# Kernel tuning notes

Hardware: AMD Instinct MI355X
Metric: run time of the kernel (lower is better)

The kernel has to match this reference:

```python
import jax, jax.numpy as jnp
import numpy as np

N_NODES = 100000
N_EDGES = 1600000
N_FEAT = 128
HIDDEN = 64
N_CLASSES = 16


def setup_inputs() -> dict:
    key = jax.random.key(0)
    ks = jax.random.split(key, 8)
    x = jax.random.normal(ks[0], (N_NODES, N_FEAT), dtype=jnp.float32)
    edge_index = jax.random.randint(ks[1], (2, N_EDGES), 0, N_NODES, dtype=jnp.int64)
    def glorot(k, shape):
        lim = float(np.sqrt(6.0 / (shape[0] + shape[1])))
        return jax.random.uniform(k, shape, jnp.float32, -lim, lim)
    return {
        "x": x,
        "edge_index": edge_index,
        "W0": glorot(ks[2], (N_FEAT, HIDDEN)), "b0": jnp.zeros((HIDDEN,), jnp.float32),
        "W1": glorot(ks[3], (HIDDEN, HIDDEN)), "b1": jnp.zeros((HIDDEN,), jnp.float32),
        "W2": glorot(ks[4], (HIDDEN, 2)),      "b2": jnp.zeros((2,), jnp.float32),
        "Wc": glorot(ks[5], (2, N_CLASSES)),   "bc": jnp.zeros((N_CLASSES,), jnp.float32),
    }


def _gcn_conv(x, W, b, src, dst, norm, n_nodes):
    # GCNConv: D^{-1/2} (A + I) D^{-1/2} X W + b, edges already include self-loops
    h = x @ W                                  # transform first (small dim)
    msg = h[src] * norm[:, None]               # gather + per-edge scale
    agg = jax.ops.segment_sum(msg, dst, num_segments=n_nodes)  # scatter-add
    return agg + b


def reference(x, edge_index, W0, b0, W1, b1, W2, b2, Wc, bc):
    n = x.shape[0]
    loops = jnp.arange(n, dtype=edge_index.dtype)
    src = jnp.concatenate([edge_index[0], loops])
    dst = jnp.concatenate([edge_index[1], loops])
    # degree on destination (col), including self-loops
    deg = jax.ops.segment_sum(jnp.ones_like(dst, dtype=x.dtype), dst, num_segments=n)
    dis = jnp.where(deg > 0, jax.lax.rsqrt(deg), 0.0)
    norm = dis[src] * dis[dst]

    h = _gcn_conv(x, W0, b0, src, dst, norm, n)              # layer 0, no activation
    h = jnp.tanh(_gcn_conv(h, W1, b1, src, dst, norm, n))    # layer 1
    h = jnp.tanh(_gcn_conv(h, W2, b2, src, dst, norm, n))    # layer 2 -> [N, 2]
    embeddings = h
    out = embeddings @ Wc + bc                               # [N, num_classes]
    return (out, embeddings)
```

## Files before the change

kernel.cpp:

```cpp
#include <hip/hip_runtime.h>


#define NF 128
#define NH 64
#define NPB 256
#define MAXNB 512
#define CAP 6144
#define A1G 1024

__global__ void k_init0(const int* __restrict__ ei, int* __restrict__ fmt,
                        int* __restrict__ ccnt, int nb16) {
    int i = blockIdx.x * 256 + threadIdx.x;
    if (i < nb16) ccnt[i] = 0;
    if (i == 0) {
        int f = 1;
        #pragma unroll
        for (int k = 1; k < 32; k += 2) if (ei[k] != 0) f = 0;
        *fmt = f;
    }
}

__global__ void __launch_bounds__(256) k_coarse(
        const int* __restrict__ ei, const int* __restrict__ fmt,
        int* __restrict__ ccnt, int* __restrict__ blockbase, int E, int NB) {
    __shared__ int h[MAXNB];
    int sh = *fmt;
    for (int i = threadIdx.x; i < NB; i += 256) h[i] = 0;
    __syncthreads();
    for (long long e = (long long)blockIdx.x * 256 + threadIdx.x; e < E;
         e += (long long)A1G * 256) {
        int d = ei[(long long)(E + e) << sh];
        atomicAdd(&h[d >> 8], 1);
    }
    __syncthreads();
    for (int b = threadIdx.x; b < NB; b += 256) {
        int c = h[b];
        int base = (c > 0) ? atomicAdd(&ccnt[b * 16], c) : 0;
        blockbase[(long long)blockIdx.x * NB + b] = base;
    }
}

__global__ void __launch_bounds__(512) k_cscan(
        const int* __restrict__ ccnt, int* __restrict__ cstart, int NB) {
    __shared__ int s[512];
    int t = threadIdx.x;
    int c = (t < NB) ? ccnt[t * 16] : 0;
    s[t] = c;
    __syncthreads();
    for (int off = 1; off < 512; off <<= 1) {
        int v = s[t];
        int u = (t >= off) ? s[t - off] : 0;
        __syncthreads();
        s[t] = v + u;
        __syncthreads();
    }
    if (t < NB) cstart[t] = s[t] - c;
}

__global__ void __launch_bounds__(256) k_cscatter(
        const int* __restrict__ ei, const int* __restrict__ fmt,
        const int* __restrict__ cstart, const int* __restrict__ blockbase,
        int* __restrict__ pairs, int E, int NB) {
    __shared__ int h[MAXNB];
    __shared__ int bb[MAXNB];
    int sh = *fmt;
    for (int i = threadIdx.x; i < NB; i += 256) {
        h[i] = 0;
        bb[i] = cstart[i] + blockbase[(long long)blockIdx.x * NB + i];
    }
    __syncthreads();
    for (long long e = (long long)blockIdx.x * 256 + threadIdx.x; e < E;
         e += (long long)A1G * 256) {
        int s = ei[(long long)e << sh];
        int d = ei[(long long)(E + e) << sh];
        int b = d >> 8;
        int r = atomicAdd(&h[b], 1);
        pairs[bb[b] + r] = s | ((d & 255) << 17);
    }
}

__global__ void __launch_bounds__(256) k_bucket(
        const int* __restrict__ pairs, const int* __restrict__ ccnt,
        const int* __restrict__ cstart, int* __restrict__ esrc,
        int* __restrict__ cnt, int* __restrict__ start, float* __restrict__ dis,
        int N) {
    __shared__ int words[CAP];
    __shared__ unsigned char rk[CAP];
    __shared__ int h[NPB];
    __shared__ int hs[NPB];
    int b = blockIdx.x;
    int cs = cstart[b];
    int ec = ccnt[b * 16];
    if (ec > CAP) ec = CAP;
    int t = threadIdx.x;
    for (int i = t; i < ec; i += 256) words[i] = pairs[cs + i];
    h[t] = 0;
    __syncthreads();
    for (int i = t; i < ec; i += 256) {
        int ld = words[i] >> 17;
        rk[i] = (unsigned char)atomicAdd(&h[ld], 1);
    }
    __syncthreads();
    int c = h[t];
    hs[t] = c;
    __syncthreads();
    for (int off = 1; off < 256; off <<= 1) {
        int v = hs[t];
        int u = (t >= off) ? hs[t - off] : 0;
        __syncthreads();
        hs[t] = v + u;
        __syncthreads();
    }
    int node = b * NPB + t;
    if (node < N) {
        cnt[node] = c;
        start[node] = cs + hs[t] - c;
        dis[node] = rsqrtf(1.0f + (float)c);
    }
    for (int i = t; i < ec; i += 256) {
        int w = words[i];
        int ld = w >> 17;
        esrc[cs + (hs[ld] - h[ld]) + rk[i]] = w & 0x1FFFF;
    }
}

template<int K>
__global__ void __launch_bounds__(256) k_gemm(
        const float* __restrict__ X, const float* __restrict__ W,
        const float* __restrict__ dis, short* __restrict__ T16,
        float* __restrict__ rs, int n) {
    constexpr int KP = K + 4;
    __shared__ float xs[64 * KP];
    __shared__ float Ws[K * NH];
    __shared__ int rmax[64];
    if (threadIdx.x < 64) rmax[threadIdx.x] = 0;
    for (int i = threadIdx.x; i < K * NH / 4; i += 256)
        ((float4*)Ws)[i] = ((const float4*)W)[i];
    long long rowbase = (long long)blockIdx.x * 64;
    const float4* X4 = (const float4*)(X + rowbase * K);
    long long lim4 = ((long long)n * K - rowbase * K) >> 2;
    for (int i = threadIdx.x; i < 16 * K; i += 256) {
        float4 v = (i < lim4) ? X4[i] : make_float4(0.f, 0.f, 0.f, 0.f);
        int r = i / (K / 4), kk = (i % (K / 4)) * 4;
        *(float4*)&xs[r * KP + kk] = v;
    }
    __syncthreads();
    int c0 = (threadIdx.x & 15) * 4;
    int r0 = (threadIdx.x >> 4) * 4;
    const float* x0 = &xs[(r0 + 0) * KP];
    const float* x1 = &xs[(r0 + 1) * KP];
    const float* x2 = &xs[(r0 + 2) * KP];
    const float* x3 = &xs[(r0 + 3) * KP];
    float4 a0{0,0,0,0}, a1{0,0,0,0}, a2{0,0,0,0}, a3{0,0,0,0};
    #pragma unroll 4
    for (int k4 = 0; k4 < K / 4; ++k4) {
        float4 xv0 = *(const float4*)(x0 + k4 * 4);
        float4 xv1 = *(const float4*)(x1 + k4 * 4);
        float4 xv2 = *(const float4*)(x2 + k4 * 4);
        float4 xv3 = *(const float4*)(x3 + k4 * 4);
        float4 wa = *(const float4*)&Ws[(k4 * 4 + 0) * NH + c0];
        float4 wb = *(const float4*)&Ws[(k4 * 4 + 1) * NH + c0];
        float4 wc = *(const float4*)&Ws[(k4 * 4 + 2) * NH + c0];
        float4 wd = *(const float4*)&Ws[(k4 * 4 + 3) * NH + c0];
        a0.x += xv0.x * wa.x; a0.y += xv0.x * wa.y; a0.z += xv0.x * wa.z; a0.w += xv0.x * wa.w;
        a1.x += xv1.x * wa.x; a1.y += xv1.x * wa.y; a1.z += xv1.x * wa.z; a1.w += xv1.x * wa.w;
        a2.x += xv2.x * wa.x; a2.y += xv2.x * wa.y; a2.z += xv2.x * wa.z; a2.w += xv2.x * wa.w;
        a3.x += xv3.x * wa.x; a3.y += xv3.x * wa.y; a3.z += xv3.x * wa.z; a3.w += xv3.x * wa.w;
        a0.x += xv0.y * wb.x; a0.y += xv0.y * wb.y; a0.z += xv0.y * wb.z; a0.w += xv0.y * wb.w;
        a1.x += xv1.y * wb.x; a1.y += xv1.y * wb.y; a1.z += xv1.y * wb.z; a1.w += xv1.y * wb.w;
        a2.x += xv2.y * wb.x; a2.y += xv2.y * wb.y; a2.z += xv2.y * wb.z; a2.w += xv2.y * wb.w;
        a3.x += xv3.y * wb.x; a3.y += xv3.y * wb.y; a3.z += xv3.y * wb.z; a3.w += xv3.y * wb.w;
        a0.x += xv0.z * wc.x; a0.y += xv0.z * wc.y; a0.z += xv0.z * wc.z; a0.w += xv0.z * wc.w;
        a1.x += xv1.z * wc.x; a1.y += xv1.z * wc.y; a1.z += xv1.z * wc.z; a1.w += xv1.z * wc.w;
        a2.x += xv2.z * wc.x; a2.y += xv2.z * wc.y; a2.z += xv2.z * wc.z; a2.w += xv2.z * wc.w;
        a3.x += xv3.z * wc.x; a3.y += xv3.z * wc.y; a3.z += xv3.z * wc.z; a3.w += xv3.z * wc.w;
        a0.x += xv0.w * wd.x; a0.y += xv0.w * wd.y; a0.z += xv0.w * wd.z; a0.w += xv0.w * wd.w;
        a1.x += xv1.w * wd.x; a1.y += xv1.w * wd.y; a1.z += xv1.w * wd.z; a1.w += xv1.w * wd.w;
        a2.x += xv2.w * wd.x; a2.y += xv2.w * wd.y; a2.z += xv2.w * wd.z; a2.w += xv2.w * wd.w;
        a3.x += xv3.w * wd.x; a3.y += xv3.w * wd.y; a3.z += xv3.w * wd.z; a3.w += xv3.w * wd.w;
    }
    int row = (int)rowbase + r0;
    float d0 = (row + 0 < n) ? dis[row + 0] : 0.0f;
    float d1 = (row + 1 < n) ? dis[row + 1] : 0.0f;
    float d2 = (row + 2 < n) ? dis[row + 2] : 0.0f;
    float d3 = (row + 3 < n) ? dis[row + 3] : 0.0f;
    a0.x *= d0; a0.y *= d0; a0.z *= d0; a0.w *= d0;
    a1.x *= d1; a1.y *= d1; a1.z *= d1; a1.w *= d1;
    a2.x *= d2; a2.y *= d2; a2.z *= d2; a2.w *= d2;
    a3.x *= d3; a3.y *= d3; a3.z *= d3; a3.w *= d3;
    float m0 = fmaxf(fmaxf(fabsf(a0.x), fabsf(a0.y)), fmaxf(fabsf(a0.z), fabsf(a0.w)));
    float m1 = fmaxf(fmaxf(fabsf(a1.x), fabsf(a1.y)), fmaxf(fabsf(a1.z), fabsf(a1.w)));
    float m2 = fmaxf(fmaxf(fabsf(a2.x), fabsf(a2.y)), fmaxf(fabsf(a2.z), fabsf(a2.w)));
    float m3 = fmaxf(fmaxf(fabsf(a3.x), fabsf(a3.y)), fmaxf(fabsf(a3.z), fabsf(a3.w)));
    atomicMax(&rmax[r0 + 0], __float_as_int(m0));
    atomicMax(&rmax[r0 + 1], __float_as_int(m1));
    atomicMax(&rmax[r0 + 2], __float_as_int(m2));
    atomicMax(&rmax[r0 + 3], __float_as_int(m3));
    __syncthreads();
    float M0 = __int_as_float(rmax[r0 + 0]);
    float M1 = __int_as_float(rmax[r0 + 1]);
    float M2 = __int_as_float(rmax[r0 + 2]);
    float M3 = __int_as_float(rmax[r0 + 3]);
    float i0 = 32767.0f / fmaxf(M0, 1e-20f);
    float i1 = 32767.0f / fmaxf(M1, 1e-20f);
    float i2 = 32767.0f / fmaxf(M2, 1e-20f);
    float i3 = 32767.0f / fmaxf(M3, 1e-20f);
    const float ks = 1.0f / 32767.0f;
    if (row + 0 < n) {
        short4 q = { (short)__float2int_rn(a0.x * i0), (short)__float2int_rn(a0.y * i0),
                     (short)__float2int_rn(a0.z * i0), (short)__float2int_rn(a0.w * i0) };
        *(short4*)&T16[(long long)(row + 0) * NH + c0] = q;
        if (c0 == 0) rs[row + 0] = M0 * ks;
    }
    if (row + 1 < n) {
        short4 q = { (short)__float2int_rn(a1.x * i1), (short)__float2int_rn(a1.y * i1),
                     (short)__float2int_rn(a1.z * i1), (short)__float2int_rn(a1.w * i1) };
        *(short4*)&T16[(long long)(row + 1) * NH + c0] = q;
        if (c0 == 0) rs[row + 1] = M1 * ks;
    }
    if (row + 2 < n) {
        short4 q = { (short)__float2int_rn(a2.x * i2), (short)__float2int_rn(a2.y * i2),
                     (short)__float2int_rn(a2.z * i2), (short)__float2int_rn(a2.w * i2) };
        *(short4*)&T16[(long long)(row + 2) * NH + c0] = q;
        if (c0 == 0) rs[row + 2] = M2 * ks;
    }
    if (row + 3 < n) {
        short4 q = { (short)__float2int_rn(a3.x * i3), (short)__float2int_rn(a3.y * i3),
                     (short)__float2int_rn(a3.z * i3), (short)__float2int_rn(a3.w * i3) };
        *(short4*)&T16[(long long)(row + 3) * NH + c0] = q;
        if (c0 == 0) rs[row + 3] = M3 * ks;
    }
}

#define EDGE_A(J) {                                                           \
    int s_ = __builtin_amdgcn_readlane(sA, (J));                              \
    float f_ = __int_as_float(__builtin_amdgcn_readlane(fAb, (J)));           \
    accA = fmaf(f_, (float)(T + s_ * NH)[lane], accA); }
#define EDGE_B(J) {                                                           \
    int s_ = __builtin_amdgcn_readlane(sB, (J));                              \
    float f_ = __int_as_float(__builtin_amdgcn_readlane(fBb, (J)));           \
    accB = fmaf(f_, (float)(T + s_ * NH)[lane], accB); }

#define SEG_GATHER2                                                           \
    int lane = threadIdx.x & 63;                                              \
    int na = blockIdx.x * 8 + (threadIdx.x >> 6) * 2;                         \
    int nb_ = na + 1;                                                         \
    if (na >= n) return;                                                      \
    bool hasB = (nb_ < n);                                                    \
    float dia = dis[na];                                                      \
    float dib = hasB ? dis[nb_] : 0.0f;                                       \
    int ga = cnt[na], sta = start[na];                                        \
    int gb = hasB ? cnt[nb_] : 0;                                             \
    int stb = hasB ? start[nb_] : 0;                                          \
    float accA = rs[na] * (float)T[na * NH + lane];                           \
    float accB = hasB ? rs[nb_] * (float)T[nb_ * NH + lane] : 0.0f;           \
    int gmax = ga > gb ? ga : gb;                                             \
    for (int base = 0; base < gmax; base += 64) {                             \
        int ma = ga - base; ma = ma < 0 ? 0 : (ma > 64 ? 64 : ma);            \
        int mb = gb - base; mb = mb < 0 ? 0 : (mb > 64 ? 64 : mb);            \
        int sA = 0, sB = 0; float fA = 0.0f, fB = 0.0f;                       \
        if (lane < ma) { sA = esrc[sta + base + lane]; fA = rs[sA]; }         \
        if (lane < mb) { sB = esrc[stb + base + lane]; fB = rs[sB]; }         \
        int fAb = __float_as_int(fA), fBb = __float_as_int(fB);               \
        int mmin = ma < mb ? ma : mb;                                         \
        int j = 0;                                                            \
        for (; j + 3 < mmin; j += 4) {                                        \
            EDGE_A(j + 0) EDGE_B(j + 0)                                       \
            EDGE_A(j + 1) EDGE_B(j + 1)                                       \
            EDGE_A(j + 2) EDGE_B(j + 2)                                       \
            EDGE_A(j + 3) EDGE_B(j + 3)                                       \
        }                                                                     \
        int jA = j, jB = j;                                                   \
        for (; jA + 3 < ma; jA += 4) {                                        \
            EDGE_A(jA + 0) EDGE_A(jA + 1) EDGE_A(jA + 2) EDGE_A(jA + 3)       \
        }                                                                     \
        for (; jA < ma; ++jA) EDGE_A(jA)                                      \
        for (; jB + 3 < mb; jB += 4) {                                        \
            EDGE_B(jB + 0) EDGE_B(jB + 1) EDGE_B(jB + 2) EDGE_B(jB + 3)       \
        }                                                                     \
        for (; jB < mb; ++jB) EDGE_B(jB)                                      \
    }

__global__ void __launch_bounds__(256) k_seg(
        const short* __restrict__ T, const float* __restrict__ rs,
        const int* __restrict__ esrc, const int* __restrict__ start,
        const int* __restrict__ cnt, const float* __restrict__ dis,
        const float* __restrict__ b, float* __restrict__ O, int n) {
    SEG_GATHER2
    float bv = b[lane];
    O[(long long)na * NH + lane] = dia * accA + bv;
    if (hasB) O[(long long)nb_ * NH + lane] = dib * accB + bv;
}

__global__ void __launch_bounds__(256) k_seg1f(
        const short* __restrict__ T, const float* __restrict__ rs,
        const int* __restrict__ esrc, const int* __restrict__ start,
        const int* __restrict__ cnt, const float* __restrict__ dis,
        const float* __restrict__ b1, const float* __restrict__ W2,
        float2* __restrict__ t2, int n) {
    SEG_GATHER2
    float bv = b1[lane];
    float2 w = ((const float2*)W2)[lane];
    float tA = tanhf(dia * accA + bv);
    float p0 = tA * w.x, p1 = tA * w.y;
    float tB = hasB ? tanhf(dib * accB + bv) : 0.0f;
    float q0 = tB * w.x, q1 = tB * w.y;
    #pragma unroll
    for (int msk = 32; msk; msk >>= 1) {
        p0 += __shfl_xor(p0, msk, 64);
        p1 += __shfl_xor(p1, msk, 64);
        q0 += __shfl_xor(q0, msk, 64);
        q1 += __shfl_xor(q1, msk, 64);
    }
    if (lane == 0) {
        t2[na] = make_float2(dia * p0, dia * p1);
        if (hasB) t2[nb_] = make_float2(dib * q0, dib * q1);
    }
}

__global__ void __launch_bounds__(256) k_seg2f(
        const float2* __restrict__ T2, const int* __restrict__ esrc,
        const int* __restrict__ start, const int* __restrict__ cnt,
        const float* __restrict__ dis, const float* __restrict__ b2,
        const float* __restrict__ Wc, const float* __restrict__ bc,
        float* __restrict__ out, float* __restrict__ emb, int n) {
    __shared__ float Wcs[32];
    __shared__ float bcs[16];
    if (threadIdx.x < 32) Wcs[threadIdx.x] = Wc[threadIdx.x];
    if (threadIdx.x < 16) bcs[threadIdx.x] = bc[threadIdx.x];
    __syncthreads();
    int i = blockIdx.x * 256 + threadIdx.x;
    if (i >= n) return;
    float di = dis[i];
    int g = cnt[i], st = start[i];
    float2 self = T2[i];
    float a0 = self.x, a1 = self.y;
    int j = 0;
    for (; j + 7 < g; j += 8) {
        int e0 = esrc[st+j],   e1 = esrc[st+j+1], e2 = esrc[st+j+2], e3 = esrc[st+j+3];
        int e4 = esrc[st+j+4], e5 = esrc[st+j+5], e6 = esrc[st+j+6], e7 = esrc[st+j+7];
        float2 v0 = T2[e0], v1 = T2[e1], v2 = T2[e2], v3 = T2[e3];
        float2 v4 = T2[e4], v5 = T2[e5], v6 = T2[e6], v7 = T2[e7];
        a0 += v0.x + v1.x + v2.x + v3.x + v4.x + v5.x + v6.x + v7.x;
        a1 += v0.y + v1.y + v2.y + v3.y + v4.y + v5.y + v6.y + v7.y;
    }
    for (; j < g; ++j) {
        float2 v = T2[esrc[st + j]];
        a0 += v.x; a1 += v.y;
    }
    float e0 = tanhf(a0 * di + b2[0]);
    float e1 = tanhf(a1 * di + b2[1]);
    *(float2*)&emb[(long long)i * 2] = make_float2(e0, e1);
    float* op = &out[(long long)i * 16];
    #pragma unroll
    for (int c4 = 0; c4 < 4; ++c4) {
        float4 o;
        o.x = e0 * Wcs[c4*4+0] + e1 * Wcs[16 + c4*4+0] + bcs[c4*4+0];
        o.y = e0 * Wcs[c4*4+1] + e1 * Wcs[16 + c4*4+1] + bcs[c4*4+1];
        o.z = e0 * Wcs[c4*4+2] + e1 * Wcs[16 + c4*4+2] + bcs[c4*4+2];
        o.w = e0 * Wcs[c4*4+3] + e1 * Wcs[16 + c4*4+3] + bcs[c4*4+3];
        *(float4*)&op[c4 * 4] = o;
    }
}

extern "C" void kernel_launch(void* const* d_in, const int* in_sizes, int n_in,
                              void* d_out, int out_size, void* d_ws, size_t ws_size,
                              hipStream_t stream) {
    const float* x  = (const float*)d_in[0];
    const int*   ei = (const int*)  d_in[1];
    const float* W0 = (const float*)d_in[2];
    const float* b0 = (const float*)d_in[3];
    const float* W1 = (const float*)d_in[4];
    const float* b1 = (const float*)d_in[5];
    const float* W2 = (const float*)d_in[6];
    const float* b2 = (const float*)d_in[7];
    const float* Wc = (const float*)d_in[8];
    const float* bc = (const float*)d_in[9];

    int N = in_sizes[0] / NF;
    int E = in_sizes[1] / 2;
    int NB = (N + NPB - 1) / NPB;

    float* out = (float*)d_out;
    float* emb = out + (long long)N * 16;

    short* T16    = (short*)d_ws;
    float* Bb     = (float*)((char*)d_ws + (long long)N * NH * 2);
    float* dis    = Bb + (long long)N * NH;
    float* rs     = dis + N;
    int*   cnt    = (int*)(rs + N);
    int*   start  = cnt + N;
    int*   esrc   = start + N;
    int*   fmt    = esrc + E;
    float2* t2    = (float2*)Bb;

    int* pairs     = (int*)d_ws;
    int* blockbase = pairs + E;
    int* ccnt      = blockbase + (long long)A1G * NB;
    int* cstart    = ccnt + NB * 16;

    int nb_n  = (N + 255) / 256;
    int nb_g  = (N + 63) / 64;
    int nb_s2 = (N + 7) / 8;
    int nb_i0 = (NB * 16 + 255) / 256;

    k_init0   <<<nb_i0, 256, 0, stream>>>(ei, fmt, ccnt, NB * 16);
    k_coarse  <<<A1G, 256, 0, stream>>>(ei, fmt, ccnt, blockbase, E, NB);
    k_cscan   <<<1, 512, 0, stream>>>(ccnt, cstart, NB);
    k_cscatter<<<A1G, 256, 0, stream>>>(ei, fmt, cstart, blockbase, pairs, E, NB);
    k_bucket  <<<NB, 256, 0, stream>>>(pairs, ccnt, cstart, esrc, cnt, start, dis, N);

    k_gemm<NF><<<nb_g, 256, 0, stream>>>(x, W0, dis, T16, rs, N);
    k_seg     <<<nb_s2, 256, 0, stream>>>(T16, rs, esrc, start, cnt, dis, b0, Bb, N);

    k_gemm<NH><<<nb_g, 256, 0, stream>>>(Bb, W1, dis, T16, rs, N);
    k_seg1f   <<<nb_s2, 256, 0, stream>>>(T16, rs, esrc, start, cnt, dis, b1, W2,
                                          t2, N);

    k_seg2f   <<<nb_n, 256, 0, stream>>>(t2, esrc, start, cnt, dis, b2, Wc, bc,
                                         out, emb, N);
}
```

Baseline: 334.2 us.

## Fuse layer-1 transform into layer-0 aggregation and split GEMM K-loop in halves

The layer-0 aggregation kernel now multiplies its result by W1 directly, using register-held W1 columns and cross-lane readlane broadcasts. It then quantizes the output to int16 with a per-row scale, so the fp32 intermediate write/read and the separate second GEMM launch are removed. The first GEMM stages X in two 64-column phases, which halves the shared-memory tile to raise occupancy at the cost of an extra barrier. The fused kernel adds 64 registers per thread for W1 and 128 readlane ops per wave, which may hurt occupancy of the gather.

```diff
diff --git a/kernel.cpp b/kernel.cpp
--- a/kernel.cpp
+++ b/kernel.cpp
@@ -124,60 +124,65 @@
     }
 }
 
-template<int K>
-__global__ void __launch_bounds__(256) k_gemm(
+#define KP2 66
+__global__ void __launch_bounds__(256) k_gemm128(
         const float* __restrict__ X, const float* __restrict__ W,
         const float* __restrict__ dis, short* __restrict__ T16,
         float* __restrict__ rs, int n) {
-    constexpr int KP = K + 4;
-    __shared__ float xs[64 * KP];
-    __shared__ float Ws[K * NH];
+    __shared__ float xs[64 * KP2];
+    __shared__ float Ws[NF * NH];
     __shared__ int rmax[64];
     if (threadIdx.x < 64) rmax[threadIdx.x] = 0;
-    for (int i = threadIdx.x; i < K * NH / 4; i += 256)
+    for (int i = threadIdx.x; i < NF * NH / 4; i += 256)
         ((float4*)Ws)[i] = ((const float4*)W)[i];
     long long rowbase = (long long)blockIdx.x * 64;
-    const float4* X4 = (const float4*)(X + rowbase * K);
-    long long lim4 = ((long long)n * K - rowbase * K) >> 2;
-    for (int i = threadIdx.x; i < 16 * K; i += 256) {
-        float4 v = (i < lim4) ? X4[i] : make_float4(0.f, 0.f, 0.f, 0.f);
-        int r = i / (K / 4), kk = (i % (K / 4)) * 4;
-        *(float4*)&xs[r * KP + kk] = v;
-    }
-    __syncthreads();
     int c0 = (threadIdx.x & 15) * 4;
     int r0 = (threadIdx.x >> 4) * 4;
-    const float* x0 = &xs[(r0 + 0) * KP];
-    const float* x1 = &xs[(r0 + 1) * KP];
-    const float* x2 = &xs[(r0 + 2) * KP];
-    const float* x3 = &xs[(r0 + 3) * KP];
     float4 a0{0,0,0,0}, a1{0,0,0,0}, a2{0,0,0,0}, a3{0,0,0,0};
-    #pragma unroll 4
-    for (int k4 = 0; k4 < K / 4; ++k4) {
-        float4 xv0 = *(const float4*)(x0 + k4 * 4);
-        float4 xv1 = *(const float4*)(x1 + k4 * 4);
-        float4 xv2 = *(const float4*)(x2 + k4 * 4);
-        float4 xv3 = *(const float4*)(x3 + k4 * 4);
-        float4 wa = *(const float4*)&Ws[(k4 * 4 + 0) * NH + c0];
-        float4 wb = *(const float4*)&Ws[(k4 * 4 + 1) * NH + c0];
-        float4 wc = *(const float4*)&Ws[(k4 * 4 + 2) * NH + c0];
-        float4 wd = *(const float4*)&Ws[(k4 * 4 + 3) * NH + c0];
-        a0.x += xv0.x * wa.x; a0.y += xv0.x * wa.y; a0.z += xv0.x * wa.z; a0.w += xv0.x * wa.w;
-        a1.x += xv1.x * wa.x; a1.y += xv1.x * wa.y; a1.z += xv1.x * wa.z; a1.w += xv1.x * wa.w;
-        a2.x += xv2.x * wa.x; a2.y += xv2.x * wa.y; a2.z += xv2.x * wa.z; a2.w += xv2.x * wa.w;
-        a3.x += xv3.x * wa.x; a3.y += xv3.x * wa.y; a3.z += xv3.x * wa.z; a3.w += xv3.x * wa.w;
-        a0.x += xv0.y * wb.x; a0.y += xv0.y * wb.y; a0.z += xv0.y * wb.z; a0.w += xv0.y * wb.w;
-        a1.x += xv1.y * wb.x; a1.y += xv1.y * wb.y; a1.z += xv1.y * wb.z; a1.w += xv1.y * wb.w;
-        a2.x += xv2.y * wb.x; a2.y += xv2.y * wb.y; a2.z += xv2.y * wb.z; a2.w += xv2.y * wb.w;
-        a3.x += xv3.y * wb.x; a3.y += xv3.y * wb.y; a3.z += xv3.y * wb.z; a3.w += xv3.y * wb.w;
-        a0.x += xv0.z * wc.x; a0.y += xv0.z * wc.y; a0.z += xv0.z * wc.z; a0.w += xv0.z * wc.w;
-        a1.x += xv1.z * wc.x; a1.y += xv1.z * wc.y; a1.z += xv1.z * wc.z; a1.w += xv1.z * wc.w;
-        a2.x += xv2.z * wc.x; a2.y += xv2.z * wc.y; a2.z += xv2.z * wc.z; a2.w += xv2.z * wc.w;
-        a3.x += xv3.z * wc.x; a3.y += xv3.z * wc.y; a3.z += xv3.z * wc.z; a3.w += xv3.z * wc.w;
-        a0.x += xv0.w * wd.x; a0.y += xv0.w * wd.y; a0.z += xv0.w * wd.z; a0.w += xv0.w * wd.w;
-        a1.x += xv1.w * wd.x; a1.y += xv1.w * wd.y; a1.z += xv1.w * wd.z; a1.w += xv1.w * wd.w;
-        a2.x += xv2.w * wd.x; a2.y += xv2.w * wd.y; a2.z += xv2.w * wd.z; a2.w += xv2.w * wd.w;
-        a3.x += xv3.w * wd.x; a3.y += xv3.w * wd.y; a3.z += xv3.w * wd.z; a3.w += xv3.w * wd.w;
+    #pragma unroll
+    for (int ph = 0; ph < 2; ++ph) {
+        if (ph) __syncthreads();
+        const float* Xp = X + rowbase * NF + ph * 64;
+        for (int i = threadIdx.x; i < 1024; i += 256) {
+            int r = i >> 4, kk = (i & 15) << 2;
+            float4 v = (rowbase + r < n)
+                           ? *(const float4*)(Xp + r * NF + kk)
+                           : make_float4(0.f, 0.f, 0.f, 0.f);
+            *(float4*)&xs[r * KP2 + kk] = v;
+        }
+        __syncthreads();
+        const float* x0 = &xs[(r0 + 0) * KP2];
+        const float* x1 = &xs[(r0 + 1) * KP2];
+        const float* x2 = &xs[(r0 + 2) * KP2];
+        const float* x3 = &xs[(r0 + 3) * KP2];
+        const float* Wp0 = &Ws[ph * 64 * NH + c0];
+        #pragma unroll 4
+        for (int k4 = 0; k4 < 16; ++k4) {
+            float4 xv0 = *(const float4*)(x0 + k4 * 4);
+            float4 xv1 = *(const float4*)(x1 + k4 * 4);
+            float4 xv2 = *(const float4*)(x2 + k4 * 4);
+            float4 xv3 = *(const float4*)(x3 + k4 * 4);
+            float4 wa = *(const float4*)(Wp0 + (k4 * 4 + 0) * NH);
+            float4 wb = *(const float4*)(Wp0 + (k4 * 4 + 1) * NH);
+            float4 wc = *(const float4*)(Wp0 + (k4 * 4 + 2) * NH);
+            float4 wd = *(const float4*)(Wp0 + (k4 * 4 + 3) * NH);
+            a0.x += xv0.x * wa.x; a0.y += xv0.x * wa.y; a0.z += xv0.x * wa.z; a0.w += xv0.x * wa.w;
+            a1.x += xv1.x * wa.x; a1.y += xv1.x * wa.y; a1.z += xv1.x * wa.z; a1.w += xv1.x * wa.w;
+            a2.x += xv2.x * wa.x; a2.y += xv2.x * wa.y; a2.z += xv2.x * wa.z; a2.w += xv2.x * wa.w;
+            a3.x += xv3.x * wa.x; a3.y += xv3.x * wa.y; a3.z += xv3.x * wa.z; a3.w += xv3.x * wa.w;
+            a0.x += xv0.y * wb.x; a0.y += xv0.y * wb.y; a0.z += xv0.y * wb.z; a0.w += xv0.y * wb.w;
+            a1.x += xv1.y * wb.x; a1.y += xv1.y * wb.y; a1.z += xv1.y * wb.z; a1.w += xv1.y * wb.w;
+            a2.x += xv2.y * wb.x; a2.y += xv2.y * wb.y; a2.z += xv2.y * wb.z; a2.w += xv2.y * wb.w;
+            a3.x += xv3.y * wb.x; a3.y += xv3.y * wb.y; a3.z += xv3.y * wb.z; a3.w += xv3.y * wb.w;
+            a0.x += xv0.z * wc.x; a0.y += xv0.z * wc.y; a0.z += xv0.z * wc.z; a0.w += xv0.z * wc.w;
+            a1.x += xv1.z * wc.x; a1.y += xv1.z * wc.y; a1.z += xv1.z * wc.z; a1.w += xv1.z * wc.w;
+            a2.x += xv2.z * wc.x; a2.y += xv2.z * wc.y; a2.z += xv2.z * wc.z; a2.w += xv2.z * wc.w;
+            a3.x += xv3.z * wc.x; a3.y += xv3.z * wc.y; a3.z += xv3.z * wc.z; a3.w += xv3.z * wc.w;
+            a0.x += xv0.w * wd.x; a0.y += xv0.w * wd.y; a0.z += xv0.w * wd.z; a0.w += xv0.w * wd.w;
+            a1.x += xv1.w * wd.x; a1.y += xv1.w * wd.y; a1.z += xv1.w * wd.z; a1.w += xv1.w * wd.w;
+            a2.x += xv2.w * wd.x; a2.y += xv2.w * wd.y; a2.z += xv2.w * wd.z; a2.w += xv2.w * wd.w;
+            a3.x += xv3.w * wd.x; a3.y += xv3.w * wd.y; a3.z += xv3.w * wd.z; a3.w += xv3.w * wd.w;
+        }
     }
     int row = (int)rowbase + r0;
     float d0 = (row + 0 < n) ? dis[row + 0] : 0.0f;
@@ -281,15 +286,44 @@
         for (; jB < mb; ++jB) EDGE_B(jB)                                      \
     }
 
-__global__ void __launch_bounds__(256) k_seg(
+__global__ void __launch_bounds__(256) k_seg0t(
         const short* __restrict__ T, const float* __restrict__ rs,
         const int* __restrict__ esrc, const int* __restrict__ start,
         const int* __restrict__ cnt, const float* __restrict__ dis,
-        const float* __restrict__ b, float* __restrict__ O, int n) {
+        const float* __restrict__ b0, const float* __restrict__ W1,
+        short* __restrict__ To, float* __restrict__ rso, int n) {
     SEG_GATHER2
-    float bv = b[lane];
-    O[(long long)na * NH + lane] = dia * accA + bv;
-    if (hasB) O[(long long)nb_ * NH + lane] = dib * accB + bv;
+    float w1r[64];
+    #pragma unroll
+    for (int c = 0; c < 64; ++c) w1r[c] = W1[c * NH + lane];
+    float bv = b0[lane];
+    float hA = dia * accA + bv;
+    float hB = dib * accB + bv;
+    float oA = 0.0f, oB = 0.0f;
+    #pragma unroll
+    for (int c = 0; c < 64; ++c) {
+        float ha = __int_as_float(__builtin_amdgcn_readlane(__float_as_int(hA), c));
+        float hb = __int_as_float(__builtin_amdgcn_readlane(__float_as_int(hB), c));
+        oA = fmaf(ha, w1r[c], oA);
+        oB = fmaf(hb, w1r[c], oB);
+    }
+    oA *= dia;
+    oB *= dib;
+    float mA = fabsf(oA), mB = fabsf(oB);
+    #pragma unroll
+    for (int msk = 32; msk; msk >>= 1) {
+        mA = fmaxf(mA, __shfl_xor(mA, msk, 64));
+        mB = fmaxf(mB, __shfl_xor(mB, msk, 64));
+    }
+    float iA = 32767.0f / fmaxf(mA, 1e-20f);
+    float iB = 32767.0f / fmaxf(mB, 1e-20f);
+    const float ks = 1.0f / 32767.0f;
+    To[(long long)na * NH + lane] = (short)__float2int_rn(oA * iA);
+    if (lane == 0) rso[na] = mA * ks;
+    if (hasB) {
+        To[(long long)nb_ * NH + lane] = (short)__float2int_rn(oB * iB);
+        if (lane == 0) rso[nb_] = mB * ks;
+    }
 }
 
 __global__ void __launch_bounds__(256) k_seg1f(
@@ -384,15 +418,17 @@
     float* out = (float*)d_out;
     float* emb = out + (long long)N * 16;
 
-    short* T16    = (short*)d_ws;
-    float* Bb     = (float*)((char*)d_ws + (long long)N * NH * 2);
-    float* dis    = Bb + (long long)N * NH;
-    float* rs     = dis + N;
-    int*   cnt    = (int*)(rs + N);
-    int*   start  = cnt + N;
-    int*   esrc   = start + N;
-    int*   fmt    = esrc + E;
-    float2* t2    = (float2*)Bb;
+    short*  T16a = (short*)d_ws;
+    char*   r2   = (char*)d_ws + (long long)N * NH * 2;
+    short*  T16b = (short*)r2;
+    float2* t2   = (float2*)(r2 + (long long)N * NH * 2);
+    float*  rs_b = (float*)(r2 + (long long)N * NH * 2 + (long long)N * 8);
+    float*  dis  = (float*)((char*)d_ws + (long long)N * NH * 2 + (long long)N * NH * 4);
+    float*  rs_a = dis + N;
+    int*    cnt   = (int*)(rs_a + N);
+    int*    start = cnt + N;
+    int*    esrc  = start + N;
+    int*    fmt   = esrc + E;
 
     int* pairs     = (int*)d_ws;
     int* blockbase = pairs + E;
@@ -410,12 +446,13 @@
     k_cscatter<<<A1G, 256, 0, stream>>>(ei, fmt, cstart, blockbase, pairs, E, NB);
     k_bucket  <<<NB, 256, 0, stream>>>(pairs, ccnt, cstart, esrc, cnt, start, dis, N);
 
-    k_gemm<NF><<<nb_g, 256, 0, stream>>>(x, W0, dis, T16, rs, N);
-    k_seg     <<<nb_s2, 256, 0, stream>>>(T16, rs, esrc, start, cnt, dis, b0, Bb, N);
-
-    k_gemm<NH><<<nb_g, 256, 0, stream>>>(Bb, W1, dis, T16, rs, N);
-    k_seg1f   <<<nb_s2, 256, 0, stream>>>(T16, rs, esrc, start, cnt, dis, b1, W2,
-                                          t2, N);
+    k_gemm128 <<<nb_g, 256, 0, stream>>>(x, W0, dis, T16a, rs_a, N);
+
+    k_seg0t   <<<nb_s2, 256, 0, stream>>>(T16a, rs_a, esrc, start, cnt, dis, b0,
+                                          W1, T16b, rs_b, N);
+
+    k_seg1f   <<<nb_s2, 256, 0, stream>>>(T16b, rs_b, esrc, start, cnt, dis, b1,
+                                          W2, t2, N);
 
     k_seg2f   <<<nb_n, 256, 0, stream>>>(t2, esrc, start, cnt, dis, b2, Wc, bc,
                                          out, emb, N);
```

Result: slower. 375.7 us (+12.4%).
